# Performance work log

Hardware: AMD Instinct MI355X
Metric: run time of the kernel (lower is better)

## Reference

```python
import jax, jax.numpy as jnp
import numpy as np

NUM_HEADS = 8
ROPE_THETA = 10.0


def _axial_angles(height, width, head_dim, theta):
    # frequencies: 1/theta^(arange(0, head_dim, 4)[:head_dim//4] / head_dim)  -> [head_dim//4]
    hd4 = head_dim // 4
    freqs = 1.0 / (theta ** (np.arange(0, head_dim, 4)[:hd4].astype(np.float32) / head_dim))
    t = np.arange(height * width)
    t_x = (t % width).astype(np.float32)
    t_y = (t // width).astype(np.float32)
    ang_x = np.outer(t_x, freqs)  # [n, head_dim//4]
    ang_y = np.outer(t_y, freqs)
    return jnp.asarray(ang_x), jnp.asarray(ang_y)


def _apply_rope(x, cos, sin):
    # x: [b, h, n, half]; cos/sin: [n, half//2]; complex-pair rotation on last dim
    xr = x[..., 0::2]
    xi = x[..., 1::2]
    out_r = xr * cos - xi * sin
    out_i = xr * sin + xi * cos
    return jnp.stack([out_r, out_i], axis=-1).reshape(x.shape)


def setup_inputs() -> dict:
    key = jax.random.key(0)
    ks = jax.random.split(key, 5)
    b, n, c = 4, 16384, 512
    x = jax.random.normal(ks[0], (b, n, c), dtype=jnp.float32)
    w_qkv = jax.random.normal(ks[1], (c, 3 * c), dtype=jnp.float32) * 0.02
    b_qkv = jax.random.normal(ks[2], (3 * c,), dtype=jnp.float32) * 0.02
    w_proj = jax.random.normal(ks[3], (c, c), dtype=jnp.float32) * 0.02
    b_proj = jax.random.normal(ks[4], (c,), dtype=jnp.float32) * 0.02
    return {"x": x, "w_qkv": w_qkv, "b_qkv": b_qkv, "w_proj": w_proj, "b_proj": b_proj,
            "height": 128, "width": 128}


def reference(x, w_qkv, b_qkv, w_proj, b_proj, height, width):
    b, n, c = x.shape
    h = NUM_HEADS
    hd = c // h
    half = hd // 2

    qkv = (x @ w_qkv + b_qkv).reshape(b, n, 3, h, hd).transpose(2, 0, 3, 1, 4)
    q, k, v = qkv[0], qkv[1], qkv[2]  # each [b, h, n, hd]

    ang_x, ang_y = _axial_angles(height, width, hd, ROPE_THETA)
    cx, sx = jnp.cos(ang_x), jnp.sin(ang_x)
    cy, sy = jnp.cos(ang_y), jnp.sin(ang_y)

    q = jnp.concatenate([_apply_rope(q[..., :half], cx, sx),
                         _apply_rope(q[..., half:], cy, sy)], axis=-1)
    k = jnp.concatenate([_apply_rope(k[..., :half], cx, sx),
                         _apply_rope(k[..., half:], cy, sy)], axis=-1)

    # kernel feature map: elu(x) + 1 (positive)
    q = jax.nn.elu(q) + 1.0
    k = jax.nn.elu(k) + 1.0

    # linear attention: O(n d^2)
    kv = jnp.einsum('bhnd,bhne->bhde', k, v)
    out = jnp.einsum('bhnd,bhde->bhne', q, kv)
    z = 1.0 / (jnp.einsum('bhnd,bhd->bhn', q, k.sum(axis=2)) + 1e-6)
    out = out * z[..., None]

    out = out.transpose(0, 2, 1, 3).reshape(b, n, c)
    return out @ w_proj + b_proj
```

## Files before the change

### kernel.cpp

```cpp
#include <hip/hip_runtime.h>
#include <math.h>

#define BATCH 4
#define NTOK  16384
#define CDIM  512
#define NH    8
#define HD    64
#define M_ROWS (BATCH*NTOK)
#define KDIM  512

typedef _Float16 f16;
typedef _Float16 f16x8 __attribute__((ext_vector_type(8)));
typedef _Float16 f16x4 __attribute__((ext_vector_type(4)));
typedef _Float16 f16x2 __attribute__((ext_vector_type(2)));
typedef float    f32x4 __attribute__((ext_vector_type(4)));

__device__ __forceinline__ void load_lds16(const void* g, void* l) {
    __builtin_amdgcn_global_load_lds(
        (const __attribute__((address_space(1))) void*)g,
        (__attribute__((address_space(3))) void*)l, 16, 0, 0);
}

__global__ void rope_tables(float* __restrict__ tab) {
    int tid = threadIdx.x;
    for (int i = 0; i < 32; i++) {
        int idx = tid + i * 256;
        int grp = idx >> 11;
        int rem = idx & 2047;
        int t   = rem >> 4;
        int fi  = rem & 15;
        float freq_f = (float)pow(10.0, -(double)fi / 16.0);
        double ang = (double)t * (double)freq_f;
        tab[idx] = (float)((grp & 1) ? sin(ang) : cos(ang));
    }
}

__global__ void convert_x_f16(const float* __restrict__ in, f16* __restrict__ outp) {
    int i = blockIdx.x * 256 + threadIdx.x;
    float4 a = *(const float4*)&in[(size_t)i * 8];
    float4 b = *(const float4*)&in[(size_t)i * 8 + 4];
    f16x8 o;
    o[0]=(f16)a.x; o[1]=(f16)a.y; o[2]=(f16)a.z; o[3]=(f16)a.w;
    o[4]=(f16)b.x; o[5]=(f16)b.y; o[6]=(f16)b.z; o[7]=(f16)b.w;
    *(f16x8*)&outp[(size_t)i * 8] = o;
}

__global__ void convert_wT(const float* __restrict__ w, f16* __restrict__ wt, int N) {
    int idx = blockIdx.x * 256 + threadIdx.x;
    int n = idx >> 9, k = idx & 511;
    wt[idx] = (f16)w[(size_t)k * N + n];
}

template<int MODE>
__global__ __launch_bounds__(256, 2)
void gemm_f16(const f16* __restrict__ A, const f16* __restrict__ Bt,
              const float* __restrict__ bias,
              float* __restrict__ Co,
              f16* __restrict__ qd, f16* __restrict__ kd, f16* __restrict__ vd,
              const float* __restrict__ tab, int ncol_tiles)
{
    __shared__ f16 As[128 * 64];
    __shared__ f16 Bs[128 * 64];
    const int tid  = threadIdx.x;
    const int lane = tid & 63;
    const int wave = tid >> 6;
    const int wy = wave >> 1, wx = wave & 1;

    const int bid = blockIdx.x;
    const int xcd = bid & 7;
    const int idx = bid >> 3;
    const int ct  = idx % ncol_tiles;
    const int rt  = (idx / ncol_tiles) * 8 + xcd;
    const int row0 = rt * 128;
    const int col0 = ct * 128;

    const int l15 = lane & 15;
    const int l4  = lane >> 4;

    f32x4 acc[4][4];
    #pragma unroll
    for (int mt = 0; mt < 4; mt++)
        #pragma unroll
        for (int nt = 0; nt < 4; nt++)
            acc[mt][nt] = (f32x4){0.f, 0.f, 0.f, 0.f};

    const int pbase = wave * 256;

    for (int k0 = 0; k0 < KDIM; k0 += 64) {
        #pragma unroll
        for (int i = 0; i < 4; i++) {
            int p  = pbase + i * 64 + lane;
            int m  = p >> 3;
            int jp = p & 7;
            int j  = jp ^ (m & 7);
            load_lds16(&A [(size_t)(row0 + m) * KDIM + k0 + j * 8],
                       &As[(pbase + i * 64) * 8]);
            load_lds16(&Bt[(size_t)(col0 + m) * KDIM + k0 + j * 8],
                       &Bs[(pbase + i * 64) * 8]);
        }
        __syncthreads();

        #pragma unroll
        for (int s = 0; s < 2; s++) {
            f16x8 af[4], bf[4];
            #pragma unroll
            for (int t = 0; t < 4; t++) {
                int ra = wy * 64 + t * 16 + l15;
                int rb = wx * 64 + t * 16 + l15;
                int ca = ((s << 2) | l4) ^ (ra & 7);
                int cb = ((s << 2) | l4) ^ (rb & 7);
                af[t] = *(const f16x8*)&As[ra * 64 + ca * 8];
                bf[t] = *(const f16x8*)&Bs[rb * 64 + cb * 8];
            }
            #pragma unroll
            for (int mt = 0; mt < 4; mt++)
                #pragma unroll
                for (int nt = 0; nt < 4; nt++)
                    acc[mt][nt] = __builtin_amdgcn_mfma_f32_16x16x32_f16(af[mt], bf[nt], acc[mt][nt], 0, 0, 0);
        }
        __syncthreads();
    }

    if (MODE == 0) {
        float* ep = (float*)&As[0];
        #pragma unroll
        for (int mt = 0; mt < 4; mt++) {
            #pragma unroll
            for (int nt = 0; nt < 4; nt++) {
                int col = wx * 64 + nt * 16 + l15;
                float bv = bias[col0 + col];
                #pragma unroll
                for (int r = 0; r < 4; r++) {
                    int rp = wy * 16 + l4 * 4 + r;
                    ep[rp * 128 + col] = acc[mt][nt][r] + bv;
                }
            }
            __syncthreads();
            #pragma unroll
            for (int j = 0; j < 4; j++) {
                int id = tid + j * 256;
                int rp = id >> 5, c4 = id & 31;
                int grow = row0 + (rp >> 4) * 64 + mt * 16 + (rp & 15);
                float4 v4 = *(const float4*)&ep[rp * 128 + c4 * 4];
                *(float4*)&Co[(size_t)grow * CDIM + col0 + c4 * 4] = v4;
            }
            __syncthreads();
        }
    } else {
        const int which = col0 >> 9;
        f16* dst = (which == 0) ? qd : (which == 1) ? kd : vd;
        #pragma unroll
        for (int nt = 0; nt < 4; nt++) {
            int coln = col0 + wx * 64 + nt * 16 + l15;
            int c512 = coln & 511;
            float bv = bias[coln];
            if (which == 2) {
                #pragma unroll
                for (int mt = 0; mt < 4; mt++)
                    #pragma unroll
                    for (int r = 0; r < 4; r++) {
                        int row = row0 + wy * 64 + mt * 16 + l4 * 4 + r;
                        float val = acc[mt][nt][r] + bv;
                        float pv  = __shfl_xor(val, 1, 64);
                        if (!(lane & 1)) {
                            f16x2 pk; pk[0] = (f16)val; pk[1] = (f16)pv;
                            *(f16x2*)&dst[(size_t)row * CDIM + c512] = pk;
                        }
                    }
            } else {
                int ch  = c512 & 63;
                int isy = ch >> 5;
                int fid = (ch & 31) >> 1;
                const float* ctb = tab + (isy ? 4096 : 0)    + fid;
                const float* stb = tab + (isy ? 6144 : 2048) + fid;
                #pragma unroll
                for (int mt = 0; mt < 4; mt++)
                    #pragma unroll
                    for (int r = 0; r < 4; r++) {
                        int row = row0 + wy * 64 + mt * 16 + l4 * 4 + r;
                        int tok = row & (NTOK - 1);
                        int t   = isy ? (tok >> 7) : (tok & 127);
                        float c = ctb[t * 16], s = stb[t * 16];
                        float val = acc[mt][nt][r] + bv;
                        float pv  = __shfl_xor(val, 1, 64);
                        float xr = (lane & 1) ? pv  : val;
                        float xi = (lane & 1) ? val : pv;
                        float o_r = xr * c - xi * s;
                        float o_i = xr * s + xi * c;
                        o_r = (o_r > 0.f) ? o_r + 1.f : __expf(o_r);
                        o_i = (o_i > 0.f) ? o_i + 1.f : __expf(o_i);
                        if (!(lane & 1)) {
                            f16x2 pk; pk[0] = (f16)o_r; pk[1] = (f16)o_i;
                            *(f16x2*)&dst[(size_t)row * CDIM + c512] = pk;
                        }
                    }
            }
        }
    }
}

__global__ __launch_bounds__(256, 4)
void kv_kernel(const f16* __restrict__ kk, const f16* __restrict__ vv,
               float* __restrict__ kv, float* __restrict__ ksum)
{
    int bh = blockIdx.x;
    int b = bh >> 3, h = bh & 7;
    int t0 = blockIdx.y * 1024;
    __shared__ float ks[64][68];
    __shared__ float vs[64][68];
    int tid = threadIdx.x;
    int tx = tid & 15;
    int ty = tid >> 4;
    float acc[4][4];
    float ksacc[4];
    #pragma unroll
    for (int r = 0; r < 4; r++) { ksacc[r] = 0.f;
        #pragma unroll
        for (int j = 0; j < 4; j++) acc[r][j] = 0.f; }

    const size_t rowbase = (size_t)b * NTOK;
    for (int tt = t0; tt < t0 + 1024; tt += 64) {
        #pragma unroll
        for (int i = 0; i < 2; i++) {
            int idx = tid + i * 256;
            int tok = idx >> 3;
            int o   = (idx & 7) * 8;
            size_t g = (rowbase + tt + tok) * CDIM + h * HD + o;
            f16x8 k8 = *(const f16x8*)&kk[g];
            f16x8 v8 = *(const f16x8*)&vv[g];
            float4 klo = {(float)k8[0], (float)k8[1], (float)k8[2], (float)k8[3]};
            float4 khi = {(float)k8[4], (float)k8[5], (float)k8[6], (float)k8[7]};
            float4 vlo = {(float)v8[0], (float)v8[1], (float)v8[2], (float)v8[3]};
            float4 vhi = {(float)v8[4], (float)v8[5], (float)v8[6], (float)v8[7]};
            *(float4*)&ks[tok][o]     = klo;
            *(float4*)&ks[tok][o + 4] = khi;
            *(float4*)&vs[tok][o]     = vlo;
            *(float4*)&vs[tok][o + 4] = vhi;
        }
        __syncthreads();
        #pragma unroll 8
        for (int t = 0; t < 64; t++) {
            float4 kd4 = *(const float4*)&ks[t][ty * 4];
            float4 vd4 = *(const float4*)&vs[t][tx * 4];
            float ka[4] = {kd4.x, kd4.y, kd4.z, kd4.w};
            float va[4] = {vd4.x, vd4.y, vd4.z, vd4.w};
            #pragma unroll
            for (int r = 0; r < 4; r++) {
                ksacc[r] += ka[r];
                #pragma unroll
                for (int j = 0; j < 4; j++) acc[r][j] += ka[r] * va[j];
            }
        }
        __syncthreads();
    }
    #pragma unroll
    for (int r = 0; r < 4; r++)
        #pragma unroll
        for (int j = 0; j < 4; j++)
            atomicAdd(&kv[bh * 4096 + (ty * 4 + r) * 64 + tx * 4 + j], acc[r][j]);
    if (tx == 0) {
        #pragma unroll
        for (int r = 0; r < 4; r++) atomicAdd(&ksum[bh * 64 + ty * 4 + r], ksacc[r]);
    }
}

__global__ __launch_bounds__(256, 4)
void attn_kernel(const f16* __restrict__ q, const float* __restrict__ kv,
                 const float* __restrict__ ksum, f16* __restrict__ attnh)
{
    int bh = blockIdx.x;
    int b = bh >> 3, h = bh & 7;
    int rc = blockIdx.y;
    __shared__ float kvs[64][68];
    __shared__ float qs[64][68];
    __shared__ float ksums[64];
    __shared__ float zpart[64][4];
    __shared__ float zs[64];
    int tid = threadIdx.x;
    int tx = tid & 15;
    int ty = tid >> 4;

    #pragma unroll
    for (int i = 0; i < 4; i++) {
        int idx = tid + i * 256;
        *(float4*)&kvs[idx >> 4][(idx & 15) * 4] = *(const float4*)&kv[bh * 4096 + idx * 4];
    }
    if (tid < 64) ksums[tid] = ksum[bh * 64 + tid];

    for (int sub = 0; sub < 4; sub++) {
        int r0 = rc * 256 + sub * 64;
        #pragma unroll
        for (int i = 0; i < 2; i++) {
            int idx = tid + i * 256;
            int rr = idx >> 3;
            int o  = (idx & 7) * 8;
            f16x8 q8 = *(const f16x8*)&q[((size_t)b * NTOK + r0 + rr) * CDIM + h * HD + o];
            float4 lo = {(float)q8[0], (float)q8[1], (float)q8[2], (float)q8[3]};
            float4 hi = {(float)q8[4], (float)q8[5], (float)q8[6], (float)q8[7]};
            *(float4*)&qs[rr][o]     = lo;
            *(float4*)&qs[rr][o + 4] = hi;
        }
        __syncthreads();
        {
            int row = tid & 63, g = tid >> 6;
            float p = 0.f;
            #pragma unroll
            for (int d = 0; d < 16; d++) p += qs[row][g * 16 + d] * ksums[g * 16 + d];
            zpart[row][g] = p;
        }
        __syncthreads();
        if (tid < 64)
            zs[tid] = 1.f / (zpart[tid][0] + zpart[tid][1] + zpart[tid][2] + zpart[tid][3] + 1e-6f);
        __syncthreads();

        float acc[4][4];
        #pragma unroll
        for (int r = 0; r < 4; r++)
            #pragma unroll
            for (int e = 0; e < 4; e++) acc[r][e] = 0.f;

        for (int d = 0; d < 64; d += 4) {
            float qa[4][4], ka[4][4];
            #pragma unroll
            for (int r = 0; r < 4; r++) {
                float4 v4 = *(const float4*)&qs[ty * 4 + r][d];
                qa[r][0]=v4.x; qa[r][1]=v4.y; qa[r][2]=v4.z; qa[r][3]=v4.w;
            }
            #pragma unroll
            for (int j = 0; j < 4; j++) {
                float4 v4 = *(const float4*)&kvs[d + j][tx * 4];
                ka[j][0]=v4.x; ka[j][1]=v4.y; ka[j][2]=v4.z; ka[j][3]=v4.w;
            }
            #pragma unroll
            for (int r = 0; r < 4; r++)
                #pragma unroll
                for (int j = 0; j < 4; j++)
                    #pragma unroll
                    for (int e = 0; e < 4; e++)
                        acc[r][e] += qa[r][j] * ka[j][e];
        }
        #pragma unroll
        for (int r = 0; r < 4; r++) {
            float z = zs[ty * 4 + r];
            f16x4 o4;
            o4[0] = (f16)(acc[r][0] * z); o4[1] = (f16)(acc[r][1] * z);
            o4[2] = (f16)(acc[r][2] * z); o4[3] = (f16)(acc[r][3] * z);
            *(f16x4*)&attnh[((size_t)b * NTOK + r0 + ty * 4 + r) * CDIM + h * HD + tx * 4] = o4;
        }
        __syncthreads();
    }
}

extern "C" void kernel_launch(void* const* d_in, const int* in_sizes, int n_in,
                              void* d_out, int out_size, void* d_ws, size_t ws_size,
                              hipStream_t stream)
{
    const float* x      = (const float*)d_in[0];
    const float* w_qkv  = (const float*)d_in[1];
    const float* b_qkv  = (const float*)d_in[2];
    const float* w_proj = (const float*)d_in[3];
    const float* b_proj = (const float*)d_in[4];
    float* out = (float*)d_out;
    char*  ws  = (char*)d_ws;

    const size_t NCB = (size_t)M_ROWS * CDIM * sizeof(f16);
    f16*   xh   = (f16*)(ws);
    f16*   qh   = (f16*)(ws + NCB * 1);
    f16*   kh   = (f16*)(ws + NCB * 2);
    f16*   vh   = (f16*)(ws + NCB * 3);
    f16*   wqt  = (f16*)(ws + NCB * 4);
    f16*   wpt  = (f16*)(ws + NCB * 4 + (1536 * 512) * sizeof(f16));
    float* tab  = (float*)(ws + NCB * 4 + (1536 * 512 + 512 * 512) * sizeof(f16));
    float* kvp  = tab + 8192;
    float* ksum = kvp + 32 * 4096;

    hipMemsetAsync(kvp, 0, (32 * 4096 + 32 * 64) * sizeof(float), stream);
    rope_tables<<<1, 256, 0, stream>>>(tab);
    convert_x_f16<<<M_ROWS * CDIM / 8 / 256, 256, 0, stream>>>(x, xh);
    convert_wT<<<1536 * 512 / 256, 256, 0, stream>>>(w_qkv, wqt, 1536);
    convert_wT<<<512 * 512 / 256, 256, 0, stream>>>(w_proj, wpt, 512);

    gemm_f16<1><<<6144, 256, 0, stream>>>(xh, wqt, b_qkv,
                                          nullptr, qh, kh, vh, tab, 12);
    kv_kernel<<<dim3(32, 16), 256, 0, stream>>>(kh, vh, kvp, ksum);
    attn_kernel<<<dim3(32, 64), 256, 0, stream>>>(qh, kvp, ksum, vh);
    gemm_f16<0><<<2048, 256, 0, stream>>>(vh, wpt, b_proj,
                                          out, nullptr, nullptr, nullptr, nullptr, 4);
}
```

Baseline: 649.0 us.

## Use MFMA with split-f16 KV in attention and permute QKV weight columns

The attention kernel moves from a scalar fp32 LDS-tiled matmul to MFMA 16x16x32 f16 instructions. KV is split into hi and lo f16 parts so the products keep close to fp32 accuracy, and the normaliser is computed with wave shuffles. The QKV weight columns are permuted so each lane holds both members of a RoPE pair, which removes the shuffle and half-idle stores in the GEMM epilogue. The rope table is interleaved as cos/sin float2 and KV is stored transposed. This costs two MFMAs per tile plus some extra rounding error from the f16 split.

Measured after the change: 548.6 us. -15.5%, faster.

```diff
diff --git a/kernel.cpp b/kernel.cpp
--- a/kernel.cpp
+++ b/kernel.cpp
@@ -23,15 +23,14 @@
 
 __global__ void rope_tables(float* __restrict__ tab) {
     int tid = threadIdx.x;
-    for (int i = 0; i < 32; i++) {
+    for (int i = 0; i < 16; i++) {
         int idx = tid + i * 256;
-        int grp = idx >> 11;
-        int rem = idx & 2047;
-        int t   = rem >> 4;
-        int fi  = rem & 15;
-        float freq_f = (float)pow(10.0, -(double)fi / 16.0);
-        double ang = (double)t * (double)freq_f;
-        tab[idx] = (float)((grp & 1) ? sin(ang) : cos(ang));
+        int t   = (idx >> 4) & 127;
+        int fi  = idx & 15;
+        double freq = pow(10.0, -(double)fi / 16.0);
+        double ang  = (double)t * freq;
+        tab[idx * 2]     = (float)cos(ang);
+        tab[idx * 2 + 1] = (float)sin(ang);
     }
 }
 
@@ -45,10 +44,16 @@
     *(f16x8*)&outp[(size_t)i * 8] = o;
 }
 
+template<int PERM>
 __global__ void convert_wT(const float* __restrict__ w, f16* __restrict__ wt, int N) {
     int idx = blockIdx.x * 256 + threadIdx.x;
     int n = idx >> 9, k = idx & 511;
-    wt[idx] = (f16)w[(size_t)k * N + n];
+    int tc = n;
+    if (PERM) {
+        int blk = n >> 5, pos = n & 31;
+        tc = blk * 32 + ((pos < 16) ? (pos * 2) : ((pos - 16) * 2 + 1));
+    }
+    wt[idx] = (f16)w[(size_t)k * N + tc];
 }
 
 template<int MODE>
@@ -149,30 +154,28 @@
     } else {
         const int which = col0 >> 9;
         f16* dst = (which == 0) ? qd : (which == 1) ? kd : vd;
-        #pragma unroll
-        for (int nt = 0; nt < 4; nt++) {
-            int coln = col0 + wx * 64 + nt * 16 + l15;
-            int c512 = coln & 511;
-            float bv = bias[coln];
+        const float2* tab2 = (const float2*)tab;
+        #pragma unroll
+        for (int q = 0; q < 2; q++) {
+            int B32  = (col0 + wx * 64 + q * 32) >> 5;
+            int t0   = B32 * 32 + 2 * l15;
+            int c512 = t0 & 511;
+            float bv0 = bias[t0];
+            float bv1 = bias[t0 + 1];
+            int isy  = B32 & 1;
+            const float2* ct = tab2 + isy * 2048 + l15;
             if (which == 2) {
                 #pragma unroll
                 for (int mt = 0; mt < 4; mt++)
                     #pragma unroll
                     for (int r = 0; r < 4; r++) {
                         int row = row0 + wy * 64 + mt * 16 + l4 * 4 + r;
-                        float val = acc[mt][nt][r] + bv;
-                        float pv  = __shfl_xor(val, 1, 64);
-                        if (!(lane & 1)) {
-                            f16x2 pk; pk[0] = (f16)val; pk[1] = (f16)pv;
-                            *(f16x2*)&dst[(size_t)row * CDIM + c512] = pk;
-                        }
+                        f16x2 pk;
+                        pk[0] = (f16)(acc[mt][2 * q][r]     + bv0);
+                        pk[1] = (f16)(acc[mt][2 * q + 1][r] + bv1);
+                        *(f16x2*)&dst[(size_t)row * CDIM + c512] = pk;
                     }
             } else {
-                int ch  = c512 & 63;
-                int isy = ch >> 5;
-                int fid = (ch & 31) >> 1;
-                const float* ctb = tab + (isy ? 4096 : 0)    + fid;
-                const float* stb = tab + (isy ? 6144 : 2048) + fid;
                 #pragma unroll
                 for (int mt = 0; mt < 4; mt++)
                     #pragma unroll
@@ -180,19 +183,15 @@
                         int row = row0 + wy * 64 + mt * 16 + l4 * 4 + r;
                         int tok = row & (NTOK - 1);
                         int t   = isy ? (tok >> 7) : (tok & 127);
-                        float c = ctb[t * 16], s = stb[t * 16];
-                        float val = acc[mt][nt][r] + bv;
-                        float pv  = __shfl_xor(val, 1, 64);
-                        float xr = (lane & 1) ? pv  : val;
-                        float xi = (lane & 1) ? val : pv;
-                        float o_r = xr * c - xi * s;
-                        float o_i = xr * s + xi * c;
+                        float2 cs = ct[t * 16];
+                        float xr = acc[mt][2 * q][r]     + bv0;
+                        float xi = acc[mt][2 * q + 1][r] + bv1;
+                        float o_r = xr * cs.x - xi * cs.y;
+                        float o_i = xr * cs.y + xi * cs.x;
                         o_r = (o_r > 0.f) ? o_r + 1.f : __expf(o_r);
                         o_i = (o_i > 0.f) ? o_i + 1.f : __expf(o_i);
-                        if (!(lane & 1)) {
-                            f16x2 pk; pk[0] = (f16)o_r; pk[1] = (f16)o_i;
-                            *(f16x2*)&dst[(size_t)row * CDIM + c512] = pk;
-                        }
+                        f16x2 pk; pk[0] = (f16)o_r; pk[1] = (f16)o_i;
+                        *(f16x2*)&dst[(size_t)row * CDIM + c512] = pk;
                     }
             }
         }
@@ -201,7 +200,7 @@
 
 __global__ __launch_bounds__(256, 4)
 void kv_kernel(const f16* __restrict__ kk, const f16* __restrict__ vv,
-               float* __restrict__ kv, float* __restrict__ ksum)
+               float* __restrict__ kvt, float* __restrict__ ksum)
 {
     int bh = blockIdx.x;
     int b = bh >> 3, h = bh & 7;
@@ -257,7 +256,7 @@
     for (int r = 0; r < 4; r++)
         #pragma unroll
         for (int j = 0; j < 4; j++)
-            atomicAdd(&kv[bh * 4096 + (ty * 4 + r) * 64 + tx * 4 + j], acc[r][j]);
+            atomicAdd(&kvt[bh * 4096 + (tx * 4 + j) * 64 + (ty * 4 + r)], acc[r][j]);
     if (tx == 0) {
         #pragma unroll
         for (int r = 0; r < 4; r++) atomicAdd(&ksum[bh * 64 + ty * 4 + r], ksacc[r]);
@@ -265,89 +264,95 @@
 }
 
 __global__ __launch_bounds__(256, 4)
-void attn_kernel(const f16* __restrict__ q, const float* __restrict__ kv,
+void attn_kernel(const f16* __restrict__ q, const float* __restrict__ kvt,
                  const float* __restrict__ ksum, f16* __restrict__ attnh)
 {
     int bh = blockIdx.x;
     int b = bh >> 3, h = bh & 7;
     int rc = blockIdx.y;
-    __shared__ float kvs[64][68];
-    __shared__ float qs[64][68];
-    __shared__ float ksums[64];
-    __shared__ float zpart[64][4];
-    __shared__ float zs[64];
+    __shared__ f16 kvhi[64 * 64];
+    __shared__ f16 kvlo[64 * 64];
     int tid = threadIdx.x;
-    int tx = tid & 15;
-    int ty = tid >> 4;
-
-    #pragma unroll
-    for (int i = 0; i < 4; i++) {
-        int idx = tid + i * 256;
-        *(float4*)&kvs[idx >> 4][(idx & 15) * 4] = *(const float4*)&kv[bh * 4096 + idx * 4];
-    }
-    if (tid < 64) ksums[tid] = ksum[bh * 64 + tid];
-
-    for (int sub = 0; sub < 4; sub++) {
-        int r0 = rc * 256 + sub * 64;
-        #pragma unroll
-        for (int i = 0; i < 2; i++) {
-            int idx = tid + i * 256;
-            int rr = idx >> 3;
-            int o  = (idx & 7) * 8;
-            f16x8 q8 = *(const f16x8*)&q[((size_t)b * NTOK + r0 + rr) * CDIM + h * HD + o];
-            float4 lo = {(float)q8[0], (float)q8[1], (float)q8[2], (float)q8[3]};
-            float4 hi = {(float)q8[4], (float)q8[5], (float)q8[6], (float)q8[7]};
-            *(float4*)&qs[rr][o]     = lo;
-            *(float4*)&qs[rr][o + 4] = hi;
-        }
-        __syncthreads();
-        {
-            int row = tid & 63, g = tid >> 6;
-            float p = 0.f;
-            #pragma unroll
-            for (int d = 0; d < 16; d++) p += qs[row][g * 16 + d] * ksums[g * 16 + d];
-            zpart[row][g] = p;
-        }
-        __syncthreads();
-        if (tid < 64)
-            zs[tid] = 1.f / (zpart[tid][0] + zpart[tid][1] + zpart[tid][2] + zpart[tid][3] + 1e-6f);
-        __syncthreads();
-
-        float acc[4][4];
-        #pragma unroll
-        for (int r = 0; r < 4; r++)
-            #pragma unroll
-            for (int e = 0; e < 4; e++) acc[r][e] = 0.f;
-
-        for (int d = 0; d < 64; d += 4) {
-            float qa[4][4], ka[4][4];
-            #pragma unroll
-            for (int r = 0; r < 4; r++) {
-                float4 v4 = *(const float4*)&qs[ty * 4 + r][d];
-                qa[r][0]=v4.x; qa[r][1]=v4.y; qa[r][2]=v4.z; qa[r][3]=v4.w;
-            }
-            #pragma unroll
-            for (int j = 0; j < 4; j++) {
-                float4 v4 = *(const float4*)&kvs[d + j][tx * 4];
-                ka[j][0]=v4.x; ka[j][1]=v4.y; ka[j][2]=v4.z; ka[j][3]=v4.w;
-            }
-            #pragma unroll
-            for (int r = 0; r < 4; r++)
-                #pragma unroll
-                for (int j = 0; j < 4; j++)
-                    #pragma unroll
-                    for (int e = 0; e < 4; e++)
-                        acc[r][e] += qa[r][j] * ka[j][e];
-        }
+    const int lane = tid & 63;
+    const int wave = tid >> 6;
+    const int l15 = lane & 15;
+    const int l4  = lane >> 4;
+
+    {
+        int e = tid >> 2;
+        #pragma unroll
+        for (int c = 0; c < 2; c++) {
+            int chunk = (tid & 3) * 2 + c;
+            f16x8 hi8, lo8;
+            #pragma unroll
+            for (int j = 0; j < 8; j++) {
+                float v = kvt[bh * 4096 + e * 64 + chunk * 8 + j];
+                f16 hv = (f16)v;
+                hi8[j] = hv;
+                lo8[j] = (f16)(v - (float)hv);
+            }
+            int cp = chunk ^ (e & 7);
+            *(f16x8*)&kvhi[e * 64 + cp * 8] = hi8;
+            *(f16x8*)&kvlo[e * 64 + cp * 8] = lo8;
+        }
+    }
+    float ksA[2][8];
+    #pragma unroll
+    for (int s = 0; s < 2; s++)
+        #pragma unroll
+        for (int j = 0; j < 8; j++)
+            ksA[s][j] = ksum[bh * 64 + s * 32 + l4 * 8 + j];
+    __syncthreads();
+
+    f16x8 bhi[2][4], blo[2][4];
+    #pragma unroll
+    for (int s = 0; s < 2; s++)
+        #pragma unroll
+        for (int nt = 0; nt < 4; nt++) {
+            int e  = nt * 16 + l15;
+            int cp = ((s << 2) | l4) ^ (e & 7);
+            bhi[s][nt] = *(const f16x8*)&kvhi[e * 64 + cp * 8];
+            blo[s][nt] = *(const f16x8*)&kvlo[e * 64 + cp * 8];
+        }
+
+    const size_t qbase = ((size_t)b * NTOK + rc * 256 + wave * 64) * CDIM + (size_t)h * HD;
+
+    #pragma unroll
+    for (int mt = 0; mt < 4; mt++) {
+        f16x8 af[2];
+        #pragma unroll
+        for (int s = 0; s < 2; s++)
+            af[s] = *(const f16x8*)&q[qbase + (size_t)(mt * 16 + l15) * CDIM + s * 32 + l4 * 8];
+
+        float zp = 0.f;
+        #pragma unroll
+        for (int s = 0; s < 2; s++)
+            #pragma unroll
+            for (int j = 0; j < 8; j++)
+                zp += (float)af[s][j] * ksA[s][j];
+        zp += __shfl_xor(zp, 16, 64);
+        zp += __shfl_xor(zp, 32, 64);
+        float zinv = 1.f / (zp + 1e-6f);
+
+        f32x4 acc[4];
+        #pragma unroll
+        for (int nt = 0; nt < 4; nt++) acc[nt] = (f32x4){0.f, 0.f, 0.f, 0.f};
+        #pragma unroll
+        for (int s = 0; s < 2; s++)
+            #pragma unroll
+            for (int nt = 0; nt < 4; nt++) {
+                acc[nt] = __builtin_amdgcn_mfma_f32_16x16x32_f16(af[s], bhi[s][nt], acc[nt], 0, 0, 0);
+                acc[nt] = __builtin_amdgcn_mfma_f32_16x16x32_f16(af[s], blo[s][nt], acc[nt], 0, 0, 0);
+            }
+
         #pragma unroll
         for (int r = 0; r < 4; r++) {
-            float z = zs[ty * 4 + r];
-            f16x4 o4;
-            o4[0] = (f16)(acc[r][0] * z); o4[1] = (f16)(acc[r][1] * z);
-            o4[2] = (f16)(acc[r][2] * z); o4[3] = (f16)(acc[r][3] * z);
-            *(f16x4*)&attnh[((size_t)b * NTOK + r0 + ty * 4 + r) * CDIM + h * HD + tx * 4] = o4;
-        }
-        __syncthreads();
+            float zr = __shfl(zinv, l4 * 4 + r, 64);
+            size_t orow = qbase + (size_t)(mt * 16 + l4 * 4 + r) * CDIM;
+            #pragma unroll
+            for (int nt = 0; nt < 4; nt++)
+                attnh[orow + nt * 16 + l15] = (f16)(acc[nt][r] * zr);
+        }
     }
 }
 
@@ -377,8 +382,8 @@
     hipMemsetAsync(kvp, 0, (32 * 4096 + 32 * 64) * sizeof(float), stream);
     rope_tables<<<1, 256, 0, stream>>>(tab);
     convert_x_f16<<<M_ROWS * CDIM / 8 / 256, 256, 0, stream>>>(x, xh);
-    convert_wT<<<1536 * 512 / 256, 256, 0, stream>>>(w_qkv, wqt, 1536);
-    convert_wT<<<512 * 512 / 256, 256, 0, stream>>>(w_proj, wpt, 512);
+    convert_wT<1><<<1536 * 512 / 256, 256, 0, stream>>>(w_qkv, wqt, 1536);
+    convert_wT<0><<<512 * 512 / 256, 256, 0, stream>>>(w_proj, wpt, 512);
 
     gemm_f16<1><<<6144, 256, 0, stream>>>(xh, wqt, b_qkv,
                                           nullptr, qh, kh, vh, tab, 12);
```
